# Optimization experiments

Measured on AMD Instinct MI355X. Metric: run time of the kernel, lower is better.

Reference implementation:

```python
import math
import jax, jax.numpy as jnp
import numpy as np

CT = {"SDD": 1000.0, "SCD": 500.0, "det_interval": 1.0, "num_det": 736}


def ramp_filter_np(ct, scale):
    # Standard equiangular fan-beam ramp filter (utility.ramp_filter):
    #   h[0] = 1/(8*db^2); h[n odd] = -1/(2*(pi*sin(n*db))^2); h[n even!=0] = 0
    db = ct["det_interval"] / ct["SDD"] * scale  # angular detector pitch at this scale
    n_det = int(ct["num_det"] // scale)
    n = np.arange(-(n_det - 1), n_det)  # length K = 2*n_det - 1
    h = np.zeros(n.shape, dtype=np.float32)
    h[n == 0] = 1.0 / (8.0 * db ** 2)
    odd = (n % 2) != 0
    h[odd] = -0.5 / (np.pi * np.sin(n[odd] * db)) ** 2
    return h


def setup_inputs() -> dict:
    key = jax.random.key(0)
    scale = 1
    batch, ch, view, det = 16, 1, 1152, CT["num_det"] // scale
    sinogram = jax.random.normal(key, (batch, ch, view, det), dtype=jnp.float32)
    delta_b = CT["det_interval"] / CT["SDD"]
    # recon_filter = ramp_filter * scale * delta_b, shaped [1,1,1,K] (OIHW)
    filt = ramp_filter_np(CT, scale) * scale * delta_b
    recon_filter = jnp.asarray(filt, dtype=jnp.float32)[None, None, None, :]
    return {"sinogram": sinogram, "recon_filter": recon_filter, "scale": scale}


def reference(sinogram, recon_filter, scale):
    det = sinogram.shape[-1]
    # cosine fan-beam pre-weighting
    s_range = (CT["det_interval"]
               * jnp.linspace((1.0 - det) / 2.0, (det - 1.0) / 2.0, det, dtype=jnp.float32)
               * scale) / CT["SDD"]
    cos_weight = (CT["SCD"] / 10000.0) * jnp.cos(s_range)  # [det]
    x = sinogram * cos_weight[None, None, None, :]
    # 1D ramp-filter convolution along detector axis (F.conv2d with 1xK kernel)
    K = recon_filter.shape[-1]
    pad = K // 2
    out = jax.lax.conv_general_dilated(
        x, recon_filter,
        window_strides=(1, 1),
        padding=[(0, 0), (pad, pad)],
        dimension_numbers=("NCHW", "OIHW", "NCHW"),
    )
    return out
```

## Files before the change

kernel.cpp:

```cpp
#include <hip/hip_runtime.h>

typedef unsigned short ushort_t;
typedef ushort_t u16x8 __attribute__((ext_vector_type(8)));
typedef __bf16 bf16x8 __attribute__((ext_vector_type(8)));
typedef float f32x4 __attribute__((ext_vector_type(4)));

#define DET 736
#define NPAD 768
#define NT 23

__device__ __forceinline__ ushort_t f2bf(float f) {
    unsigned u = __builtin_bit_cast(unsigned, f);
    u += 0x7FFFu + ((u >> 16) & 1u);
    return (ushort_t)(u >> 16);
}

__device__ __forceinline__ void gload16(const void* g, void* l) {
    __builtin_amdgcn_global_load_lds(
        (const __attribute__((address_space(1))) unsigned int*)g,
        (__attribute__((address_space(3))) unsigned int*)l,
        16, 0, 0);
}

__global__ void prep_bt(const float* __restrict__ filt, ushort_t* __restrict__ Bt) {
    int idx = blockIdx.x * blockDim.x + threadIdx.x;
    if (idx >= NPAD * DET) return;
    int n = idx / DET;
    int k = idx - n * DET;
    float w = 0.05f * cosf(((float)k - 367.5f) * 0.001f);
    float v = (n < DET) ? filt[k - n + (DET - 1)] * w : 0.0f;
    Bt[idx] = f2bf(v);
}

__global__ __launch_bounds__(256, 3) void gemm_fused(
    const float* __restrict__ A,
    const ushort_t* __restrict__ Bt,
    float* __restrict__ C, int M)
{
    __shared__ float As[2][128 * 32];

    const int tid  = threadIdx.x;
    const int lane = tid & 63;
    const int warp = tid >> 6;
    const int wm   = warp & 1;
    const int wn   = warp >> 1;
    const int quad = lane >> 4;
    const int l16  = lane & 15;

    const size_t row_a0 = (size_t)blockIdx.x * 128;
    const int    row_b0 = blockIdx.y * 128;

    f32x4 acc[4][4];
#pragma unroll
    for (int i = 0; i < 4; ++i)
#pragma unroll
        for (int jx = 0; jx < 4; ++jx)
            acc[i][jx] = (f32x4){0.f, 0.f, 0.f, 0.f};

    const float* gsrc[4];
    int          cdst[4];
#pragma unroll
    for (int i = 0; i < 4; ++i) {
        int c    = tid + i * 256;
        int row  = c >> 3;
        int part = c & 7;
        int sp   = part ^ (row & 7);
        gsrc[i]  = A + (row_a0 + row) * DET + sp * 4;
        cdst[i]  = c * 4;
    }

    const ushort_t* gBp[4];
#pragma unroll
    for (int ni = 0; ni < 4; ++ni)
        gBp[ni] = Bt + (size_t)(row_b0 + wn * 64 + ni * 16 + l16) * DET + quad * 8;

    const int r7   = l16 & 7;
    const int o_lo = ((quad * 2)     ^ r7) * 4;
    const int o_hi = ((quad * 2 + 1) ^ r7) * 4;

#pragma unroll
    for (int i = 0; i < 4; ++i)
        gload16(gsrc[i], &As[0][cdst[i]]);
    u16x8 bcur[4];
#pragma unroll
    for (int ni = 0; ni < 4; ++ni)
        bcur[ni] = *(const u16x8*)(gBp[ni]);
    __syncthreads();

    for (int t = 0; t < NT; ++t) {
        const int cur = t & 1;
        const int kn  = (t + 1 < NT) ? (t + 1) * 32 : 0;

#pragma unroll
        for (int i = 0; i < 4; ++i)
            gload16(gsrc[i] + kn, &As[cur ^ 1][cdst[i]]);
        u16x8 bnext[4];
#pragma unroll
        for (int ni = 0; ni < 4; ++ni)
            bnext[ni] = *(const u16x8*)(gBp[ni] + kn);

        bf16x8 af[4];
#pragma unroll
        for (int mi = 0; mi < 4; ++mi) {
            const int row = wm * 64 + mi * 16 + l16;
            f32x4 lo = *(const f32x4*)(&As[cur][row * 32 + o_lo]);
            f32x4 hi = *(const f32x4*)(&As[cur][row * 32 + o_hi]);
            bf16x8 v;
#pragma unroll
            for (int e = 0; e < 4; ++e) {
                v[e]     = (__bf16)lo[e];
                v[e + 4] = (__bf16)hi[e];
            }
            af[mi] = v;
        }

#pragma unroll
        for (int mi = 0; mi < 4; ++mi)
#pragma unroll
            for (int ni = 0; ni < 4; ++ni)
                acc[mi][ni] = __builtin_amdgcn_mfma_f32_16x16x32_bf16(
                    af[mi],
                    __builtin_bit_cast(bf16x8, bcur[ni]),
                    acc[mi][ni], 0, 0, 0);

        __syncthreads();
#pragma unroll
        for (int ni = 0; ni < 4; ++ni)
            bcur[ni] = bnext[ni];
    }

#pragma unroll
    for (int mi = 0; mi < 4; ++mi) {
#pragma unroll
        for (int ni = 0; ni < 4; ++ni) {
            int colg = row_b0 + wn * 64 + ni * 16 + l16;
            if (colg < DET) {
#pragma unroll
                for (int r = 0; r < 4; ++r) {
                    size_t rowg = row_a0 + wm * 64 + mi * 16 + quad * 4 + r;
                    C[rowg * DET + colg] = acc[mi][ni][r];
                }
            }
        }
    }
}

extern "C" void kernel_launch(void* const* d_in, const int* in_sizes, int n_in,
                              void* d_out, int out_size, void* d_ws, size_t ws_size,
                              hipStream_t stream) {
    const float* sino = (const float*)d_in[0];
    const float* filt = (const float*)d_in[1];
    int total = in_sizes[0];
    int M = total / DET;

    ushort_t* Btb = (ushort_t*)d_ws;
    float* out = (float*)d_out;

    prep_bt<<<(NPAD * DET + 255) / 256, 256, 0, stream>>>(filt, Btb);

    dim3 grid(M / 128, NPAD / 128);
    gemm_fused<<<grid, 256, 0, stream>>>(sino, Btb, out, M);
}
```

Before: 146.8 us.

## Convert full A row-panel to bf16 in LDS once and stream B per warp

Result: slower. 175.5 us (+19.6%).

```diff
diff --git a/kernel.cpp b/kernel.cpp
--- a/kernel.cpp
+++ b/kernel.cpp
@@ -8,19 +8,8 @@
 #define DET 736
 #define NPAD 768
 #define NT 23
-
-__device__ __forceinline__ ushort_t f2bf(float f) {
-    unsigned u = __builtin_bit_cast(unsigned, f);
-    u += 0x7FFFu + ((u >> 16) & 1u);
-    return (ushort_t)(u >> 16);
-}
-
-__device__ __forceinline__ void gload16(const void* g, void* l) {
-    __builtin_amdgcn_global_load_lds(
-        (const __attribute__((address_space(1))) unsigned int*)g,
-        (__attribute__((address_space(3))) unsigned int*)l,
-        16, 0, 0);
-}
+#define RB 48
+#define LDW 744
 
 __global__ void prep_bt(const float* __restrict__ filt, ushort_t* __restrict__ Bt) {
     int idx = blockIdx.x * blockDim.x + threadIdx.x;
@@ -29,116 +18,104 @@
     int k = idx - n * DET;
     float w = 0.05f * cosf(((float)k - 367.5f) * 0.001f);
     float v = (n < DET) ? filt[k - n + (DET - 1)] * w : 0.0f;
-    Bt[idx] = f2bf(v);
+    Bt[idx] = __builtin_bit_cast(ushort_t, (__bf16)v);
 }
 
-__global__ __launch_bounds__(256, 3) void gemm_fused(
+__global__ __launch_bounds__(256, 2) void gemm_as(
     const float* __restrict__ A,
     const ushort_t* __restrict__ Bt,
     float* __restrict__ C, int M)
 {
-    __shared__ float As[2][128 * 32];
+    __shared__ ushort_t As[RB * LDW];
 
     const int tid  = threadIdx.x;
     const int lane = tid & 63;
     const int warp = tid >> 6;
-    const int wm   = warp & 1;
-    const int wn   = warp >> 1;
     const int quad = lane >> 4;
     const int l16  = lane & 15;
 
-    const size_t row_a0 = (size_t)blockIdx.x * 128;
-    const int    row_b0 = blockIdx.y * 128;
+    const size_t row_a0 = (size_t)blockIdx.x * RB;
 
-    f32x4 acc[4][4];
+    for (int c = tid; c < RB * 92; c += 256) {
+        int row  = c / 92;
+        int part = c - row * 92;
+        const float* g = A + (row_a0 + row) * DET + part * 8;
+        f32x4 lo = *(const f32x4*)g;
+        f32x4 hi = *(const f32x4*)(g + 4);
+        u16x8 v;
 #pragma unroll
-    for (int i = 0; i < 4; ++i)
+        for (int e = 0; e < 4; ++e) {
+            v[e]     = __builtin_bit_cast(ushort_t, (__bf16)lo[e]);
+            v[e + 4] = __builtin_bit_cast(ushort_t, (__bf16)hi[e]);
+        }
+        *(u16x8*)(As + row * LDW + part * 8) = v;
+    }
+    __syncthreads();
+
+    const int n0 = warp * 192;
+
+    for (int nc = 0; nc < 3; ++nc) {
+        const int nb = n0 + nc * 64;
+
+        f32x4 acc[3][4];
 #pragma unroll
-        for (int jx = 0; jx < 4; ++jx)
-            acc[i][jx] = (f32x4){0.f, 0.f, 0.f, 0.f};
+        for (int mi = 0; mi < 3; ++mi)
+#pragma unroll
+            for (int ni = 0; ni < 4; ++ni)
+                acc[mi][ni] = (f32x4){0.f, 0.f, 0.f, 0.f};
 
-    const float* gsrc[4];
-    int          cdst[4];
+        const ushort_t* bp[4];
 #pragma unroll
-    for (int i = 0; i < 4; ++i) {
-        int c    = tid + i * 256;
-        int row  = c >> 3;
-        int part = c & 7;
-        int sp   = part ^ (row & 7);
-        gsrc[i]  = A + (row_a0 + row) * DET + sp * 4;
-        cdst[i]  = c * 4;
-    }
+        for (int ni = 0; ni < 4; ++ni)
+            bp[ni] = Bt + (size_t)(nb + ni * 16 + l16) * DET + quad * 8;
 
-    const ushort_t* gBp[4];
+        u16x8 bcur[4], acur[3];
 #pragma unroll
-    for (int ni = 0; ni < 4; ++ni)
-        gBp[ni] = Bt + (size_t)(row_b0 + wn * 64 + ni * 16 + l16) * DET + quad * 8;
-
-    const int r7   = l16 & 7;
-    const int o_lo = ((quad * 2)     ^ r7) * 4;
-    const int o_hi = ((quad * 2 + 1) ^ r7) * 4;
+        for (int ni = 0; ni < 4; ++ni)
+            bcur[ni] = *(const u16x8*)(bp[ni]);
+#pragma unroll
+        for (int mi = 0; mi < 3; ++mi)
+            acur[mi] = *(const u16x8*)(As + (mi * 16 + l16) * LDW + quad * 8);
 
 #pragma unroll
-    for (int i = 0; i < 4; ++i)
-        gload16(gsrc[i], &As[0][cdst[i]]);
-    u16x8 bcur[4];
+        for (int t = 0; t < NT; ++t) {
+            u16x8 bnx[4], anx[3];
+            if (t + 1 < NT) {
+                const int ko = (t + 1) * 32;
 #pragma unroll
-    for (int ni = 0; ni < 4; ++ni)
-        bcur[ni] = *(const u16x8*)(gBp[ni]);
-    __syncthreads();
-
-    for (int t = 0; t < NT; ++t) {
-        const int cur = t & 1;
-        const int kn  = (t + 1 < NT) ? (t + 1) * 32 : 0;
-
+                for (int ni = 0; ni < 4; ++ni)
+                    bnx[ni] = *(const u16x8*)(bp[ni] + ko);
 #pragma unroll
-        for (int i = 0; i < 4; ++i)
-            gload16(gsrc[i] + kn, &As[cur ^ 1][cdst[i]]);
-        u16x8 bnext[4];
+                for (int mi = 0; mi < 3; ++mi)
+                    anx[mi] = *(const u16x8*)(As + (mi * 16 + l16) * LDW + ko + quad * 8);
+            }
 #pragma unroll
-        for (int ni = 0; ni < 4; ++ni)
-            bnext[ni] = *(const u16x8*)(gBp[ni] + kn);
-
-        bf16x8 af[4];
+            for (int mi = 0; mi < 3; ++mi)
 #pragma unroll
-        for (int mi = 0; mi < 4; ++mi) {
-            const int row = wm * 64 + mi * 16 + l16;
-            f32x4 lo = *(const f32x4*)(&As[cur][row * 32 + o_lo]);
-            f32x4 hi = *(const f32x4*)(&As[cur][row * 32 + o_hi]);
-            bf16x8 v;
+                for (int ni = 0; ni < 4; ++ni)
+                    acc[mi][ni] = __builtin_amdgcn_mfma_f32_16x16x32_bf16(
+                        __builtin_bit_cast(bf16x8, acur[mi]),
+                        __builtin_bit_cast(bf16x8, bcur[ni]),
+                        acc[mi][ni], 0, 0, 0);
+            if (t + 1 < NT) {
 #pragma unroll
-            for (int e = 0; e < 4; ++e) {
-                v[e]     = (__bf16)lo[e];
-                v[e + 4] = (__bf16)hi[e];
+                for (int ni = 0; ni < 4; ++ni) bcur[ni] = bnx[ni];
+#pragma unroll
+                for (int mi = 0; mi < 3; ++mi) acur[mi] = anx[mi];
             }
-            af[mi] = v;
         }
 
 #pragma unroll
-        for (int mi = 0; mi < 4; ++mi)
+        for (int mi = 0; mi < 3; ++mi) {
 #pragma unroll
-            for (int ni = 0; ni < 4; ++ni)
-                acc[mi][ni] = __builtin_amdgcn_mfma_f32_16x16x32_bf16(
-                    af[mi],
-                    __builtin_bit_cast(bf16x8, bcur[ni]),
-                    acc[mi][ni], 0, 0, 0);
-
-        __syncthreads();
+            for (int ni = 0; ni < 4; ++ni) {
+                int colg = nb + ni * 16 + l16;
+                if (colg < DET) {
 #pragma unroll
-        for (int ni = 0; ni < 4; ++ni)
-            bcur[ni] = bnext[ni];
-    }
-
-#pragma unroll
-    for (int mi = 0; mi < 4; ++mi) {
-#pragma unroll
-        for (int ni = 0; ni < 4; ++ni) {
-            int colg = row_b0 + wn * 64 + ni * 16 + l16;
-            if (colg < DET) {
-#pragma unroll
-                for (int r = 0; r < 4; ++r) {
-                    size_t rowg = row_a0 + wm * 64 + mi * 16 + quad * 4 + r;
-                    C[rowg * DET + colg] = acc[mi][ni][r];
+                    for (int r = 0; r < 4; ++r) {
+                        size_t rowg = row_a0 + mi * 16 + quad * 4 + r;
+                        C[rowg * DET + colg] = acc[mi][ni][r];
+                    }
                 }
             }
         }
@@ -158,6 +135,5 @@
 
     prep_bt<<<(NPAD * DET + 255) / 256, 256, 0, stream>>>(filt, Btb);
 
-    dim3 grid(M / 128, NPAD / 128);
-    gemm_fused<<<grid, 256, 0, stream>>>(sino, Btb, out, M);
+    gemm_as<<<dim3(M / RB), 256, 0, stream>>>(sino, Btb, out, M);
 }
```
